# Kernel optimization log

Hardware: AMD Instinct MI355X
Metric: run time of the kernel (lower is better)

Reference implementation:

```python
import jax, jax.numpy as jnp
import numpy as np
import math

N = 25000      # nodes
E = 400000     # edges
L = 2          # GAT layers
H = 8          # heads
DM = 384       # d_model
DE = 64        # d_edge
C = DM // H    # per-head out channels (48)
NB = 41        # gaussian basis: int(8.0/0.2)+1
CUTOFF = 8.0
STEP = 0.2


def setup_inputs():
    key = jax.random.key(0)
    ks = jax.random.split(key, 24)
    s = 0.05
    inp = {
        'x': jax.random.randint(ks[0], (N,), 0, 100, dtype=jnp.int32),
        'edge_index': jax.random.randint(ks[1], (2, E), 0, N, dtype=jnp.int32),
        'edge_attr': jax.random.uniform(ks[2], (E,), dtype=jnp.float32) * CUTOFF,
        'lut': jax.random.normal(ks[3], (100, DM), dtype=jnp.float32) * s,
        'We0': jax.random.normal(ks[4], (NB, DE), dtype=jnp.float32) * s,
        'be0': jnp.zeros((DE,), dtype=jnp.float32),
        'Wl': jax.random.normal(ks[5], (L, DM, DM), dtype=jnp.float32) * s,
        'bl': jnp.zeros((L, DM), dtype=jnp.float32),
        'Wr': jax.random.normal(ks[6], (L, DM, DM), dtype=jnp.float32) * s,
        'br': jnp.zeros((L, DM), dtype=jnp.float32),
        'We': jax.random.normal(ks[7], (L, DE, DM), dtype=jnp.float32) * s,
        'att': jax.random.normal(ks[8], (L, H, C), dtype=jnp.float32) * s,
        'Wres': jax.random.normal(ks[9], (L, DM, DM), dtype=jnp.float32) * s,
        'bias_g': jnp.zeros((L, DM), dtype=jnp.float32),
        'ln_g': jnp.ones((L, DM), dtype=jnp.float32),
        'ln_b': jnp.zeros((L, DM), dtype=jnp.float32),
        'bn_g': jnp.ones((DM,), dtype=jnp.float32),
        'bn_b': jnp.zeros((DM,), dtype=jnp.float32),
    }
    return inp


def _forward(x, edge_index, edge_attr, lut, We0, be0, Wl, bl, Wr, br, We,
             att, Wres, bias_g, ln_g, ln_b, bn_g, bn_b):
    # atom embedding (scaled)
    h = lut[x] * jnp.asarray(math.sqrt(DM), lut.dtype)  # [N, DM]

    # GaussianBasis + edge embedding
    values = jnp.linspace(0.0, CUTOFF, NB, dtype=edge_attr.dtype)
    diff = (edge_attr[:, None] - values) / STEP                 # [E, NB]
    basis = jnp.exp(-(diff * diff)) / 1.12
    ea = basis @ We0 + be0                                      # [E, DE]

    src0, tgt0 = edge_index[0], edge_index[1]
    # add_self_loops with fill_value='mean': scatter-mean of edge_attr at target
    cnt = jax.ops.segment_sum(jnp.ones((E,), ea.dtype), tgt0, num_segments=N)
    sums = jax.ops.segment_sum(ea, tgt0, num_segments=N)
    loop_attr = sums / jnp.maximum(cnt, 1.0)[:, None]           # [N, DE]

    loop = jnp.arange(N, dtype=src0.dtype)
    src = jnp.concatenate([src0, loop])                          # [Et]
    tgt = jnp.concatenate([tgt0, loop])
    ea_full = jnp.concatenate([ea, loop_attr], axis=0)           # [Et, DE]
    Et = E + N

    for l in range(L):
        xl = h @ Wl[l] + bl[l]                                  # [N, DM]
        xr = h @ Wr[l] + br[l]
        e_proj = ea_full @ We[l]                                # [Et, DM]
        m = (xl[src] + xr[tgt] + e_proj).reshape(Et, H, C)
        m = jax.nn.leaky_relu(m, 0.2)
        alpha = jnp.einsum('ehc,hc->eh', m, att[l])             # [Et, H]
        # segment softmax over target nodes (every node has a self-loop)
        amax = jax.ops.segment_max(alpha, tgt, num_segments=N)
        alpha = jnp.exp(alpha - amax[tgt])
        denom = jax.ops.segment_sum(alpha, tgt, num_segments=N)
        alpha = alpha / (denom[tgt] + 1e-16)
        msg = xl[src].reshape(Et, H, C) * alpha[:, :, None]
        out = jax.ops.segment_sum(msg, tgt, num_segments=N).reshape(N, DM)
        out = out + h @ Wres[l] + bias_g[l]                     # residual + bias
        # LayerNorm
        mu = out.mean(axis=-1, keepdims=True)
        var = out.var(axis=-1, keepdims=True)
        h = (out - mu) * jax.lax.rsqrt(var + 1e-5) * ln_g[l] + ln_b[l]

    # BatchNorm1d (training mode: batch stats, biased variance)
    mu = h.mean(axis=0)
    var = h.var(axis=0)
    h = (h - mu) * jax.lax.rsqrt(var + 1e-5) * bn_g + bn_b
    return h


def reference(x, edge_index, edge_attr, lut, We0, be0, Wl, bl, Wr, br, We,
              att, Wres, bias_g, ln_g, ln_b, bn_g, bn_b):
    return _forward(x, edge_index, edge_attr, lut, We0, be0, Wl, bl, Wr, br,
                    We, att, Wres, bias_g, ln_g, ln_b, bn_g, bn_b)
```

## Files before the change

### kernel.cpp

```cpp
#include <hip/hip_runtime.h>
#include <hip/hip_fp16.h>

#define DMv 384
#define DEv 64

typedef __attribute__((ext_vector_type(8))) __bf16 bf16x8;
typedef __attribute__((ext_vector_type(4))) float f32x4;
typedef _Float16 hf16x2 __attribute__((ext_vector_type(2)));

__device__ __forceinline__ float bf_lo(unsigned u){ return __uint_as_float(u << 16); }
__device__ __forceinline__ float bf_hi(unsigned u){ return __uint_as_float(u & 0xffff0000u); }
__device__ __forceinline__ unsigned short f2bf(float f){
  unsigned u = __float_as_uint(f);
  unsigned r = (u + 0x7fffu + ((u >> 16) & 1u)) >> 16;
  return (unsigned short)r;
}
__device__ __forceinline__ float bf2f(unsigned short s){ return __uint_as_float(((unsigned)s) << 16); }

__device__ __forceinline__ unsigned packh2(float a, float b){
  unsigned short ha = __half_as_ushort(__float2half(a));
  unsigned short hb = __half_as_ushort(__float2half(b));
  return (unsigned)ha | ((unsigned)hb << 16);
}
__device__ __forceinline__ float h_lo(unsigned u){ return __half2float(__ushort_as_half((unsigned short)(u & 0xffffu))); }
__device__ __forceinline__ float h_hi(unsigned u){ return __half2float(__ushort_as_half((unsigned short)(u >> 16))); }
__device__ __forceinline__ hf16x2 u2h(unsigned u){ union { unsigned u; hf16x2 h; } x; x.u = u; return x.h; }
__device__ __forceinline__ float dot2(unsigned a, unsigned b, float c){
  return __builtin_amdgcn_fdot2(u2h(a), u2h(b), c, false);
}

__device__ __forceinline__ int phi_col(int c){
  int cp = c >> 1, l = cp / 3, m = cp - 3*l;
  return ((l + (m << 6)) << 1) | (c & 1);
}

__global__ void embed_k(const int* __restrict__ x, const float* __restrict__ lut,
                        unsigned short* __restrict__ hbf) {
  int n = blockIdx.x, c = threadIdx.x;
  hbf[(size_t)n*DMv + c] = f2bf(lut[(size_t)x[n]*DMv + c] * 19.595917942265423f);
}

__global__ void w2_k(const float* __restrict__ We0, const float* __restrict__ be0,
                     const float* __restrict__ We, float* __restrict__ W2,
                     float* __restrict__ bias2) {
  int k = blockIdx.x;
  int l = blockIdx.y;
  int j = threadIdx.x;
  const float* Wel = We + (size_t)l*DEv*DMv;
  if (k == 48) {
    float s = 0.f;
    for (int c = 0; c < DEv; ++c) s = fmaf(be0[c], Wel[c*DMv + j], s);
    bias2[l*DMv + j] = s;
    return;
  }
  float s = 0.f;
  if (k < 41) {
    for (int c = 0; c < DEv; ++c) s = fmaf(We0[k*DEv + c], Wel[c*DMv + j], s);
  }
  W2[((size_t)l*48 + k)*DMv + j] = s;
}

__global__ void w2p_k(const float* __restrict__ W2, unsigned* __restrict__ W2P) {
  int p = blockIdx.x;
  int l = blockIdx.y;
  int c = threadIdx.x;
  const float* base = W2 + (size_t)l*48*DMv;
  float a = base[(2*p)*DMv + c];
  float b = base[(2*p+1)*DMv + c];
  W2P[((size_t)l*24 + p)*DMv + phi_col(c)] = packh2(a, b);
}

__global__ void wcat_k(const float* __restrict__ Wl, const float* __restrict__ Wr,
                       const float* __restrict__ Wres, unsigned short* __restrict__ WcatT) {
  int n = blockIdx.x;
  int l = blockIdx.y;
  int k = threadIdx.x;
  const float* src;
  int nn;
  if (n < 384)      { src = Wl   + (size_t)l*DMv*DMv; nn = n; }
  else if (n < 768) { src = Wr   + (size_t)l*DMv*DMv; nn = n - 384; }
  else              { src = Wres + (size_t)l*DMv*DMv; nn = n - 768; }
  WcatT[((size_t)l*1152 + n)*DMv + k] = f2bf(src[(size_t)k*DMv + nn]);
}

__global__ void bas8_k(const float* __restrict__ edge_attr,
                       uint4* __restrict__ bas8, int* __restrict__ ofs, int Ecnt) {
  int e = blockIdx.x*256 + threadIdx.x;
  if (e >= Ecnt) return;
  float d = edge_attr[e];
  int kc = (int)(d*5.0f + 0.5f);
  int s = (kc - 2) & ~3;
  if (s < 0) s = 0;
  float v[8];
  #pragma unroll
  for (int i = 0; i < 8; ++i) {
    float df = (d - 0.2f*(float)(s+i)) * 5.0f;
    v[i] = __expf(-(df*df)) * (1.0f/1.12f);
  }
  uint4 u;
  u.x = packh2(v[0], v[1]);
  u.y = packh2(v[2], v[3]);
  u.z = packh2(v[4], v[5]);
  u.w = packh2(v[6], v[7]);
  bas8[e] = u;
  ofs[e] = s;
}

__global__ void count_k(const int* __restrict__ tgt, int* __restrict__ cnt, int Ecnt) {
  int e = blockIdx.x*256 + threadIdx.x;
  if (e < Ecnt) atomicAdd(&cnt[tgt[e]], 1);
}
__global__ void scan1_k(const int* __restrict__ cnt, int* __restrict__ rowptr,
                        int* __restrict__ bsum, int n) {
  __shared__ int tmp[256];
  int tid = threadIdx.x, i = blockIdx.x*256 + tid;
  int v = (i < n) ? cnt[i] : 0;
  tmp[tid] = v; __syncthreads();
  for (int off = 1; off < 256; off <<= 1) {
    int xv = (tid >= off) ? tmp[tid-off] : 0;
    __syncthreads();
    tmp[tid] += xv;
    __syncthreads();
  }
  if (i < n) rowptr[i] = tmp[tid] - v;
  if (tid == 255) bsum[blockIdx.x] = tmp[255];
}
__global__ void scan2_k(const int* __restrict__ bsum, int* __restrict__ bsumx, int nb) {
  __shared__ int tmp[256];
  int tid = threadIdx.x;
  int v = (tid < nb) ? bsum[tid] : 0;
  tmp[tid] = v; __syncthreads();
  for (int off = 1; off < 256; off <<= 1) {
    int xv = (tid >= off) ? tmp[tid-off] : 0;
    __syncthreads();
    tmp[tid] += xv;
    __syncthreads();
  }
  bsumx[tid] = tmp[tid] - v;
}
__global__ void scan3_k(int* __restrict__ rowptr, const int* __restrict__ bsumx,
                        int n, int total) {
  int i = blockIdx.x*256 + threadIdx.x;
  if (i < n) rowptr[i] += bsumx[blockIdx.x];
  if (i == 0) rowptr[n] = total;
}
__global__ void fill_k(const int* __restrict__ srcs, const int* __restrict__ tgt,
                       const int* __restrict__ rowptr, int* __restrict__ fill,
                       const uint4* __restrict__ bas8, const int* __restrict__ ofs,
                       int* __restrict__ srcc,
                       uint4* __restrict__ bas8c, int* __restrict__ ofsc, int Ecnt) {
  int e = blockIdx.x*256 + threadIdx.x;
  if (e >= Ecnt) return;
  int t = tgt[e];
  int pos = rowptr[t] + atomicAdd(&fill[t], 1);
  srcc[pos] = srcs[e];
  ofsc[pos] = ofs[e];
  bas8c[pos] = bas8[e];
}

__global__ void mb_k(const uint4* __restrict__ bas8c, const int* __restrict__ ofsc,
                     const int* __restrict__ rowptr,
                     unsigned* __restrict__ mbpk, int Nn) {
  __shared__ float mbS[4][48];
  int tid = threadIdx.x, lane = tid & 63, wv = tid >> 6;
  int t = blockIdx.x*4 + wv;
  if (t >= Nn) return;
  if (lane < 48) mbS[wv][lane] = 0.f;
  asm volatile("s_waitcnt lgkmcnt(0)" ::: "memory");
  int rp = rowptr[t], deg = rowptr[t+1] - rp;
  for (int base = 0; base < deg; base += 64) {
    int i = base + lane;
    if (i < deg) {
      uint4 bu = bas8c[rp + i];
      int s = ofsc[rp + i];
      atomicAdd(&mbS[wv][s+0], h_lo(bu.x));
      atomicAdd(&mbS[wv][s+1], h_hi(bu.x));
      atomicAdd(&mbS[wv][s+2], h_lo(bu.y));
      atomicAdd(&mbS[wv][s+3], h_hi(bu.y));
      atomicAdd(&mbS[wv][s+4], h_lo(bu.z));
      atomicAdd(&mbS[wv][s+5], h_hi(bu.z));
      atomicAdd(&mbS[wv][s+6], h_lo(bu.w));
      atomicAdd(&mbS[wv][s+7], h_hi(bu.w));
    }
  }
  asm volatile("s_waitcnt lgkmcnt(0)" ::: "memory");
  if (lane < 24) {
    float inv = (deg > 0) ? 1.0f / (float)deg : 0.f;
    float a = (2*lane   < 44) ? mbS[wv][2*lane  ] * inv : 0.f;
    float b = (2*lane+1 < 44) ? mbS[wv][2*lane+1] * inv : 0.f;
    mbpk[(size_t)t*24 + lane] = packh2(a, b);
  }
}

__global__ __launch_bounds__(256) void mfma_cat_k(
    const unsigned short* __restrict__ Abf,
    const unsigned short* __restrict__ Bt,
    const float* __restrict__ b0, const float* __restrict__ b1, const float* __restrict__ b2,
    unsigned* __restrict__ C0h, float* __restrict__ C1, float* __restrict__ C2, int M) {
  __shared__ __align__(16) char smem[64*132*4];
  unsigned short* As = (unsigned short*)smem;
  unsigned short* Bs = (unsigned short*)(smem + 16384);
  float* Cs = (float*)smem;
  int tid = threadIdx.x;
  int lane = tid & 63, wv = tid >> 6;
  int wr = wv >> 1, wc = wv & 1;
  int bn = blockIdx.x * 128;
  int bm = blockIdx.y * 128;
  int srow = tid >> 3;
  int scol = (tid & 7) * 8;
  f32x4 acc[4][4] = {};
  uint4 av[4], bv[4];
  #pragma unroll
  for (int c = 0; c < 4; ++c) {
    int gr = bm + c*32 + srow; if (gr >= M) gr = M - 1;
    av[c] = *(const uint4*)(Abf + (size_t)gr*DMv + scol);
    bv[c] = *(const uint4*)(Bt + (size_t)(bn + c*32 + srow)*DMv + scol);
  }
  #pragma unroll
  for (int kt = 0; kt < 6; ++kt) {
    __syncthreads();
    #pragma unroll
    for (int c = 0; c < 4; ++c) {
      int r = c*32 + srow;
      int byteA = r*128 + scol*2;
      byteA ^= ((byteA >> 9) & 1) << 5;
      *(uint4*)((char*)As + byteA) = av[c];
      *(uint4*)((char*)Bs + byteA) = bv[c];
    }
    __syncthreads();
    if (kt < 5) {
      int k0 = (kt+1) * 64;
      #pragma unroll
      for (int c = 0; c < 4; ++c) {
        int gr = bm + c*32 + srow; if (gr >= M) gr = M - 1;
        av[c] = *(const uint4*)(Abf + (size_t)gr*DMv + k0 + scol);
        bv[c] = *(const uint4*)(Bt + (size_t)(bn + c*32 + srow)*DMv + k0 + scol);
      }
    }
    #pragma unroll
    for (int ks = 0; ks < 2; ++ks) {
      bf16x8 af[4], bfv[4];
      #pragma unroll
      for (int m = 0; m < 4; ++m) {
        int r = wr*64 + m*16 + (lane & 15);
        int byte = r*128 + ks*64 + ((lane >> 4)*16);
        byte ^= ((byte >> 9) & 1) << 5;
        af[m] = *(const bf16x8*)((const char*)As + byte);
      }
      #pragma unroll
      for (int n = 0; n < 4; ++n) {
        int r = wc*64 + n*16 + (lane & 15);
        int byte = r*128 + ks*64 + ((lane >> 4)*16);
        byte ^= ((byte >> 9) & 1) << 5;
        bfv[n] = *(const bf16x8*)((const char*)Bs + byte);
      }
      #pragma unroll
      for (int m = 0; m < 4; ++m)
        #pragma unroll
        for (int n = 0; n < 4; ++n)
          acc[m][n] = __builtin_amdgcn_mfma_f32_16x16x32_bf16(af[m], bfv[n], acc[m][n], 0, 0, 0);
    }
  }
  int seg = bn / 384;
  const float* bias = (seg == 0) ? b0 : (seg == 1) ? b1 : b2;
  float* C = (seg == 1) ? C1 : C2;
  int cbase = bn - seg*384;
  #pragma unroll
  for (int half = 0; half < 2; ++half) {
    __syncthreads();
    if (wr == half) {
      #pragma unroll
      for (int m = 0; m < 4; ++m) {
        int rl = m*16 + ((lane >> 4)*4);
        #pragma unroll
        for (int n = 0; n < 4; ++n) {
          int cl = wc*64 + n*16 + (lane & 15);
          #pragma unroll
          for (int q = 0; q < 4; ++q)
            Cs[(rl+q)*132 + cl] = acc[m][n][q];
        }
      }
    }
    __syncthreads();
    #pragma unroll
    for (int rep = 0; rep < 8; ++rep) {
      int rl = rep*8 + (tid >> 5);
      int c4 = (tid & 31) * 4;
      int gr = bm + half*64 + rl;
      if (gr < M) {
        float4 v = *(const float4*)&Cs[rl*132 + c4];
        float4 bv4 = *(const float4*)(bias + cbase + c4);
        v.x += bv4.x; v.y += bv4.y; v.z += bv4.z; v.w += bv4.w;
        if (seg == 0) {
          uint2 pk;
          pk.x = packh2(v.x, v.y);
          pk.y = packh2(v.z, v.w);
          *(uint2*)(C0h + (size_t)gr*192 + ((cbase + c4) >> 1)) = pk;
        } else {
          *(float4*)(C + (size_t)gr*DMv + cbase + c4) = v;
        }
      }
    }
  }
}

__global__ __launch_bounds__(256) void fused_agg_k(
    const unsigned* __restrict__ xlh, const float* __restrict__ xr,
    const float* __restrict__ hres,
    const uint4* __restrict__ bas8c, const int* __restrict__ ofsc,
    const int* __restrict__ srcc, const int* __restrict__ rowptr,
    const unsigned* __restrict__ mbpk,
    const unsigned* __restrict__ W2Pg, const float* __restrict__ bias2_l,
    const float* __restrict__ att_l,
    const float* __restrict__ ln_g, const float* __restrict__ ln_b,
    unsigned short* __restrict__ hbf, int Nn) {
  __shared__ unsigned W2P[24 * DMv];
  int tid = threadIdx.x;
  for (int i = tid; i < 24*DMv; i += 256) W2P[i] = W2Pg[i];
  __syncthreads();
  int lane = tid & 63, wv = tid >> 6;
  int j0 = lane * 6;
  float att_j[6], b2[6], lg[6], lb[6];
  #pragma unroll
  for (int jj = 0; jj < 6; ++jj) {
    att_j[jj] = att_l[j0 + jj];
    b2[jj]    = bias2_l[j0 + jj];
    lg[jj]    = ln_g[j0 + jj];
    lb[jj]    = ln_b[j0 + jj];
  }
  int wgid = blockIdx.x*4 + wv;
  for (int it = 0; it < 4; ++it) {
    int t = wgid*4 + it;
    if (t >= Nn) break;
    int rp = rowptr[t], deg = rowptr[t+1] - rp;
    const float* yp = xr + (size_t)t*DMv + j0;
    float2 c0 = ((const float2*)yp)[0], c1 = ((const float2*)yp)[1], c2 = ((const float2*)yp)[2];
    float xrr[6] = {c0.x, c0.y, c1.x, c1.y, c2.x, c2.y};
    float xrb[6];
    #pragma unroll
    for (int jj = 0; jj < 6; ++jj) xrb[jj] = xrr[jj] + b2[jj];
    float S = 0.f;
    float acc[6] = {0.f,0.f,0.f,0.f,0.f,0.f};
    int r_src = 0, r_ofs = 0; uint4 r_bu = {0,0,0,0};
    if (deg > 0 && lane < 8) {
      int idx = lane; if (idx >= deg) idx = deg - 1;
      int p = rp + idx;
      r_src = srcc[p]; r_bu = bas8c[p]; r_ofs = ofsc[p];
    }
    for (int base = 0; base < deg; base += 8) {
      int nb = deg - base; if (nb > 8) nb = 8;
      int n_src = 0, n_ofs = 0; uint4 n_bu = {0,0,0,0};
      if (base + 8 < deg && lane < 8) {
        int idx = base + 8 + lane; if (idx >= deg) idx = deg - 1;
        int p = rp + idx;
        n_src = srcc[p]; n_bu = bas8c[p]; n_ofs = ofsc[p];
      }
      float xls[8][6];
      #pragma unroll
      for (int s = 0; s < 8; ++s) {
        int sr = __shfl(r_src, s);
        const unsigned* xp = xlh + (size_t)sr*192 + lane*3;
        unsigned u0 = xp[0], u1 = xp[1], u2 = xp[2];
        xls[s][0]=h_lo(u0); xls[s][1]=h_hi(u0); xls[s][2]=h_lo(u1);
        xls[s][3]=h_hi(u1); xls[s][4]=h_lo(u2); xls[s][5]=h_hi(u2);
      }
      #pragma unroll
      for (int s = 0; s < 8; ++s) {
        if (s >= nb) break;
        int p0 = __shfl(r_ofs, s) >> 1;
        unsigned bq0 = __shfl((int)r_bu.x, s);
        unsigned bq1 = __shfl((int)r_bu.y, s);
        unsigned bq2 = __shfl((int)r_bu.z, s);
        unsigned bq3 = __shfl((int)r_bu.w, s);
        float m6[6];
        #pragma unroll
        for (int jj = 0; jj < 6; ++jj) m6[jj] = xls[s][jj] + xrb[jj];
        const uint2* row0 = (const uint2*)(W2P + (p0 + 0)*DMv);
        const uint2* row1 = (const uint2*)(W2P + (p0 + 1)*DMv);
        const uint2* row2 = (const uint2*)(W2P + (p0 + 2)*DMv);
        const uint2* row3 = (const uint2*)(W2P + (p0 + 3)*DMv);
        #pragma unroll
        for (int m = 0; m < 3; ++m) {
          uint2 w0 = row0[lane + (m << 6)];
          uint2 w1 = row1[lane + (m << 6)];
          uint2 w2 = row2[lane + (m << 6)];
          uint2 w3 = row3[lane + (m << 6)];
          m6[2*m]   = dot2(w0.x, bq0, m6[2*m]);
          m6[2*m+1] = dot2(w0.y, bq0, m6[2*m+1]);
          m6[2*m]   = dot2(w1.x, bq1, m6[2*m]);
          m6[2*m+1] = dot2(w1.y, bq1, m6[2*m+1]);
          m6[2*m]   = dot2(w2.x, bq2, m6[2*m]);
          m6[2*m+1] = dot2(w2.y, bq2, m6[2*m+1]);
          m6[2*m]   = dot2(w3.x, bq3, m6[2*m]);
          m6[2*m+1] = dot2(w3.y, bq3, m6[2*m+1]);
        }
        float part = 0.f;
        #pragma unroll
        for (int jj = 0; jj < 6; ++jj) {
          float vl = (m6[jj] > 0.f) ? m6[jj] : 0.2f*m6[jj];
          part = fmaf(vl, att_j[jj], part);
        }
        part += __shfl_xor(part, 1);
        part += __shfl_xor(part, 2);
        part += __shfl_xor(part, 4);
        float w = __expf(part);
        S += w;
        #pragma unroll
        for (int jj = 0; jj < 6; ++jj) acc[jj] = fmaf(w, xls[s][jj], acc[jj]);
      }
      r_src = n_src; r_bu = n_bu; r_ofs = n_ofs;
    }
    {
      const unsigned* xp = xlh + (size_t)t*192 + lane*3;
      unsigned u0 = xp[0], u1 = xp[1], u2 = xp[2];
      float xlt[6] = {h_lo(u0), h_hi(u0), h_lo(u1), h_hi(u1), h_lo(u2), h_hi(u2)};
      float m6[6];
      #pragma unroll
      for (int jj = 0; jj < 6; ++jj)
        m6[jj] = xlt[jj] + ((deg > 0) ? xrb[jj] : xrr[jj]);
      const uint4* mbp4 = (const uint4*)(mbpk + (size_t)t*24);
      #pragma unroll
      for (int w6 = 0; w6 < 6; ++w6) {
        uint4 bu = mbp4[w6];
        unsigned bq[4] = {bu.x, bu.y, bu.z, bu.w};
        #pragma unroll
        for (int q = 0; q < 4; ++q) {
          const uint2* rowq = (const uint2*)(W2P + (w6*4 + q)*DMv);
          #pragma unroll
          for (int m = 0; m < 3; ++m) {
            uint2 wv2 = rowq[lane + (m << 6)];
            m6[2*m]   = dot2(wv2.x, bq[q], m6[2*m]);
            m6[2*m+1] = dot2(wv2.y, bq[q], m6[2*m+1]);
          }
        }
      }
      float part = 0.f;
      #pragma unroll
      for (int jj = 0; jj < 6; ++jj) {
        float vl = (m6[jj] > 0.f) ? m6[jj] : 0.2f*m6[jj];
        part = fmaf(vl, att_j[jj], part);
      }
      part += __shfl_xor(part, 1);
      part += __shfl_xor(part, 2);
      part += __shfl_xor(part, 4);
      float w = __expf(part);
      S += w;
      #pragma unroll
      for (int jj = 0; jj < 6; ++jj) acc[jj] = fmaf(w, xlt[jj], acc[jj]);
    }
    float inv = 1.0f / (S + 1e-16f);
    const float* hrp = hres + (size_t)t*DMv + j0;
    float outv[6]; float s1 = 0.f, s2 = 0.f;
    #pragma unroll
    for (int jj = 0; jj < 6; ++jj) {
      float o = fmaf(acc[jj], inv, hrp[jj]);
      outv[jj] = o; s1 += o; s2 += o*o;
    }
    #pragma unroll
    for (int m = 1; m < 64; m <<= 1) {
      s1 += __shfl_xor(s1, m);
      s2 += __shfl_xor(s2, m);
    }
    float mu  = s1 * (1.0f/384.0f);
    float var = s2 * (1.0f/384.0f) - mu*mu;
    float rs  = rsqrtf(var + 1e-5f);
    float o0 = (outv[0]-mu)*rs*lg[0] + lb[0];
    float o1 = (outv[1]-mu)*rs*lg[1] + lb[1];
    float o2 = (outv[2]-mu)*rs*lg[2] + lb[2];
    float o3 = (outv[3]-mu)*rs*lg[3] + lb[3];
    float o4 = (outv[4]-mu)*rs*lg[4] + lb[4];
    float o5 = (outv[5]-mu)*rs*lg[5] + lb[5];
    unsigned* hp = (unsigned*)(hbf + (size_t)t*DMv + j0);
    hp[0] = (unsigned)f2bf(o0) | ((unsigned)f2bf(o1) << 16);
    hp[1] = (unsigned)f2bf(o2) | ((unsigned)f2bf(o3) << 16);
    hp[2] = (unsigned)f2bf(o4) | ((unsigned)f2bf(o5) << 16);
  }
}

__global__ void bn_reduce_k(const unsigned short* __restrict__ hbf, float* __restrict__ sums, int Nn) {
  int c = threadIdx.x;
  float s = 0.f, s2 = 0.f;
  for (int r = blockIdx.x; r < Nn; r += gridDim.x) {
    float v = bf2f(hbf[(size_t)r*DMv + c]);
    s += v; s2 += v*v;
  }
  atomicAdd(&sums[c], s);
  atomicAdd(&sums[DMv + c], s2);
}
__global__ void bn_params_k(const float* __restrict__ sums,
                            const float* __restrict__ bn_g, const float* __restrict__ bn_b,
                            float* __restrict__ scsh, int Nn) {
  int c = threadIdx.x;
  float mu  = sums[c] / (float)Nn;
  float var = sums[DMv + c] / (float)Nn - mu*mu;
  float rs  = rsqrtf(var + 1e-5f);
  float sc  = bn_g[c] * rs;
  scsh[c] = sc;
  scsh[DMv + c] = bn_b[c] - mu*sc;
}
__global__ void bn_apply_k(const unsigned short* __restrict__ hbf, const float* __restrict__ scsh,
                           float* __restrict__ out) {
  int c = threadIdx.x; int n = blockIdx.x;
  size_t i = (size_t)n*DMv + c;
  out[i] = fmaf(bf2f(hbf[i]), scsh[c], scsh[DMv + c]);
}

extern "C" void kernel_launch(void* const* d_in, const int* in_sizes, int n_in,
                              void* d_out, int out_size, void* d_ws, size_t ws_size,
                              hipStream_t stream) {
  const int Nn   = in_sizes[0];
  const int Ecnt = in_sizes[2];
  const int*   x         = (const int*)d_in[0];
  const int*   eindex    = (const int*)d_in[1];
  const int*   srcs      = eindex;
  const int*   tgts      = eindex + Ecnt;
  const float* edge_attr = (const float*)d_in[2];
  const float* lut       = (const float*)d_in[3];
  const float* We0       = (const float*)d_in[4];
  const float* be0       = (const float*)d_in[5];
  const float* Wl        = (const float*)d_in[6];
  const float* bl_       = (const float*)d_in[7];
  const float* Wr        = (const float*)d_in[8];
  const float* br_       = (const float*)d_in[9];
  const float* We        = (const float*)d_in[10];
  const float* att       = (const float*)d_in[11];
  const float* Wres      = (const float*)d_in[12];
  const float* bias_g    = (const float*)d_in[13];
  const float* ln_g      = (const float*)d_in[14];
  const float* ln_b      = (const float*)d_in[15];
  const float* bn_g      = (const float*)d_in[16];
  const float* bn_b      = (const float*)d_in[17];

  char* ws = (char*)d_ws;
  size_t off = 0;
  auto alloc = [&](size_t b) { size_t o = off; off += (b + 255) & ~(size_t)255; return o; };
  unsigned short* hbf   = (unsigned short*)(ws + alloc((size_t)Nn*DMv*2));
  unsigned* xlh = (unsigned*)(ws + alloc((size_t)Nn*192*4));
  float* xrB   = (float*)(ws + alloc((size_t)Nn*DMv*4));
  float* hresB = (float*)(ws + alloc((size_t)Nn*DMv*4));
  unsigned* mbpk = (unsigned*)(ws + alloc((size_t)Nn*24*4));
  uint4* bas8  = (uint4*)(ws + alloc((size_t)Ecnt*16));
  int* ofs     = (int*)(ws + alloc((size_t)Ecnt*4));
  uint4* bas8c = (uint4*)(ws + alloc((size_t)Ecnt*16));
  int* ofsc    = (int*)(ws + alloc((size_t)Ecnt*4));
  int* srcc    = (int*)(ws + alloc((size_t)Ecnt*4));
  float* W2    = (float*)(ws + alloc((size_t)2*48*DMv*4));
  unsigned* W2P = (unsigned*)(ws + alloc((size_t)2*24*DMv*4));
  float* bias2 = (float*)(ws + alloc((size_t)2*DMv*4));
  unsigned short* WcatT = (unsigned short*)(ws + alloc((size_t)2*1152*DMv*2));
  int* rowptr  = (int*)(ws + alloc((size_t)(Nn+1)*4));
  int* cnt     = (int*)(ws + alloc((size_t)Nn*4));
  int* fillA   = (int*)(ws + alloc((size_t)Nn*4));
  int* bsum    = (int*)(ws + alloc(1024));
  int* bsumx   = (int*)(ws + alloc(1024));
  float* bnsum = (float*)(ws + alloc(2*DMv*4));
  float* scsh  = (float*)(ws + alloc(2*DMv*4));

  hipMemsetAsync(cnt,   0, (size_t)Nn*4, stream);
  hipMemsetAsync(fillA, 0, (size_t)Nn*4, stream);
  hipMemsetAsync(bnsum, 0, 2*DMv*4, stream);

  embed_k<<<Nn, DMv, 0, stream>>>(x, lut, hbf);
  w2_k<<<dim3(49, 2), DMv, 0, stream>>>(We0, be0, We, W2, bias2);
  w2p_k<<<dim3(24, 2), DMv, 0, stream>>>(W2, W2P);
  wcat_k<<<dim3(1152, 2), DMv, 0, stream>>>(Wl, Wr, Wres, WcatT);
  bas8_k<<<(Ecnt+255)/256, 256, 0, stream>>>(edge_attr, bas8, ofs, Ecnt);
  count_k<<<(Ecnt+255)/256, 256, 0, stream>>>(tgts, cnt, Ecnt);
  int nblk = (Nn + 255)/256;
  scan1_k<<<nblk, 256, 0, stream>>>(cnt, rowptr, bsum, Nn);
  scan2_k<<<1, 256, 0, stream>>>(bsum, bsumx, nblk);
  scan3_k<<<nblk, 256, 0, stream>>>(rowptr, bsumx, Nn, Ecnt);
  fill_k<<<(Ecnt+255)/256, 256, 0, stream>>>(srcs, tgts, rowptr, fillA,
                                             bas8, ofs, srcc, bas8c, ofsc, Ecnt);
  mb_k<<<(Nn+3)/4, 256, 0, stream>>>(bas8c, ofsc, rowptr, mbpk, Nn);

  for (int l = 0; l < 2; ++l) {
    mfma_cat_k<<<dim3(9, (Nn+127)/128), 256, 0, stream>>>(
        hbf, WcatT + (size_t)l*1152*DMv,
        bl_ + (size_t)l*DMv, br_ + (size_t)l*DMv, bias_g + (size_t)l*DMv,
        xlh, xrB, hresB, Nn);
    fused_agg_k<<<(Nn+15)/16, 256, 0, stream>>>(
        xlh, xrB, hresB, bas8c, ofsc, srcc, rowptr, mbpk,
        W2P + (size_t)l*24*DMv, bias2 + (size_t)l*DMv, att + (size_t)l*DMv,
        ln_g + (size_t)l*DMv, ln_b + (size_t)l*DMv, hbf, Nn);
  }
  bn_reduce_k<<<200, DMv, 0, stream>>>(hbf, bnsum, Nn);
  bn_params_k<<<1, DMv, 0, stream>>>(bnsum, bn_g, bn_b, scsh, Nn);
  bn_apply_k<<<Nn, DMv, 0, stream>>>(hbf, scsh, (float*)d_out);
}
```

Measured before the change: 714.4 us.

## Store xr and residual GEMM outputs as fp16 and fold memsets into kernels

The GEMM epilogue now packs all three output segments (xl, xr, residual) to fp16 instead of writing xr and the residual as fp32. The aggregation kernel reads and unpacks them, halving intermediate write and read traffic per layer. The three memsets are also removed: zeroing of cnt, fillA and bnsum moves into embed_k, count_k and mb_k. This cuts launch overhead, at the cost of fp16 rounding of xr and the residual before LayerNorm.

```diff
diff --git a/kernel.cpp b/kernel.cpp
--- a/kernel.cpp
+++ b/kernel.cpp
@@ -35,8 +35,9 @@
 }
 
 __global__ void embed_k(const int* __restrict__ x, const float* __restrict__ lut,
-                        unsigned short* __restrict__ hbf) {
+                        unsigned short* __restrict__ hbf, int* __restrict__ cnt) {
   int n = blockIdx.x, c = threadIdx.x;
+  if (c == 0) cnt[n] = 0;
   hbf[(size_t)n*DMv + c] = f2bf(lut[(size_t)x[n]*DMv + c] * 19.595917942265423f);
 }
 
@@ -106,8 +107,10 @@
   ofs[e] = s;
 }
 
-__global__ void count_k(const int* __restrict__ tgt, int* __restrict__ cnt, int Ecnt) {
+__global__ void count_k(const int* __restrict__ tgt, int* __restrict__ cnt,
+                        int* __restrict__ fillA, int Ecnt, int Nn) {
   int e = blockIdx.x*256 + threadIdx.x;
+  if (e < Nn) fillA[e] = 0;
   if (e < Ecnt) atomicAdd(&cnt[tgt[e]], 1);
 }
 __global__ void scan1_k(const int* __restrict__ cnt, int* __restrict__ rowptr,
@@ -160,9 +163,11 @@
 
 __global__ void mb_k(const uint4* __restrict__ bas8c, const int* __restrict__ ofsc,
                      const int* __restrict__ rowptr,
-                     unsigned* __restrict__ mbpk, int Nn) {
+                     unsigned* __restrict__ mbpk, float* __restrict__ bnsum, int Nn) {
   __shared__ float mbS[4][48];
   int tid = threadIdx.x, lane = tid & 63, wv = tid >> 6;
+  int gid = blockIdx.x*256 + tid;
+  if (gid < 2*DMv) bnsum[gid] = 0.f;
   int t = blockIdx.x*4 + wv;
   if (t >= Nn) return;
   if (lane < 48) mbS[wv][lane] = 0.f;
@@ -196,7 +201,7 @@
     const unsigned short* __restrict__ Abf,
     const unsigned short* __restrict__ Bt,
     const float* __restrict__ b0, const float* __restrict__ b1, const float* __restrict__ b2,
-    unsigned* __restrict__ C0h, float* __restrict__ C1, float* __restrict__ C2, int M) {
+    unsigned* __restrict__ C0h, unsigned* __restrict__ C1h, unsigned* __restrict__ C2h, int M) {
   __shared__ __align__(16) char smem[64*132*4];
   unsigned short* As = (unsigned short*)smem;
   unsigned short* Bs = (unsigned short*)(smem + 16384);
@@ -263,7 +268,7 @@
   }
   int seg = bn / 384;
   const float* bias = (seg == 0) ? b0 : (seg == 1) ? b1 : b2;
-  float* C = (seg == 1) ? C1 : C2;
+  unsigned* C = (seg == 0) ? C0h : (seg == 1) ? C1h : C2h;
   int cbase = bn - seg*384;
   #pragma unroll
   for (int half = 0; half < 2; ++half) {
@@ -291,22 +296,18 @@
         float4 v = *(const float4*)&Cs[rl*132 + c4];
         float4 bv4 = *(const float4*)(bias + cbase + c4);
         v.x += bv4.x; v.y += bv4.y; v.z += bv4.z; v.w += bv4.w;
-        if (seg == 0) {
-          uint2 pk;
-          pk.x = packh2(v.x, v.y);
-          pk.y = packh2(v.z, v.w);
-          *(uint2*)(C0h + (size_t)gr*192 + ((cbase + c4) >> 1)) = pk;
-        } else {
-          *(float4*)(C + (size_t)gr*DMv + cbase + c4) = v;
-        }
+        uint2 pk;
+        pk.x = packh2(v.x, v.y);
+        pk.y = packh2(v.z, v.w);
+        *(uint2*)(C + (size_t)gr*192 + ((cbase + c4) >> 1)) = pk;
       }
     }
   }
 }
 
 __global__ __launch_bounds__(256) void fused_agg_k(
-    const unsigned* __restrict__ xlh, const float* __restrict__ xr,
-    const float* __restrict__ hres,
+    const unsigned* __restrict__ xlh, const unsigned* __restrict__ xrh,
+    const unsigned* __restrict__ hresh,
     const uint4* __restrict__ bas8c, const int* __restrict__ ofsc,
     const int* __restrict__ srcc, const int* __restrict__ rowptr,
     const unsigned* __restrict__ mbpk,
@@ -333,9 +334,9 @@
     int t = wgid*4 + it;
     if (t >= Nn) break;
     int rp = rowptr[t], deg = rowptr[t+1] - rp;
-    const float* yp = xr + (size_t)t*DMv + j0;
-    float2 c0 = ((const float2*)yp)[0], c1 = ((const float2*)yp)[1], c2 = ((const float2*)yp)[2];
-    float xrr[6] = {c0.x, c0.y, c1.x, c1.y, c2.x, c2.y};
+    const unsigned* yp = xrh + (size_t)t*192 + lane*3;
+    unsigned y0 = yp[0], y1 = yp[1], y2 = yp[2];
+    float xrr[6] = {h_lo(y0), h_hi(y0), h_lo(y1), h_hi(y1), h_lo(y2), h_hi(y2)};
     float xrb[6];
     #pragma unroll
     for (int jj = 0; jj < 6; ++jj) xrb[jj] = xrr[jj] + b2[jj];
@@ -449,11 +450,13 @@
       for (int jj = 0; jj < 6; ++jj) acc[jj] = fmaf(w, xlt[jj], acc[jj]);
     }
     float inv = 1.0f / (S + 1e-16f);
-    const float* hrp = hres + (size_t)t*DMv + j0;
+    const unsigned* hq = hresh + (size_t)t*192 + lane*3;
+    unsigned hh0 = hq[0], hh1 = hq[1], hh2 = hq[2];
+    float hr[6] = {h_lo(hh0), h_hi(hh0), h_lo(hh1), h_hi(hh1), h_lo(hh2), h_hi(hh2)};
     float outv[6]; float s1 = 0.f, s2 = 0.f;
     #pragma unroll
     for (int jj = 0; jj < 6; ++jj) {
-      float o = fmaf(acc[jj], inv, hrp[jj]);
+      float o = fmaf(acc[jj], inv, hr[jj]);
       outv[jj] = o; s1 += o; s2 += o*o;
     }
     #pragma unroll
@@ -535,9 +538,9 @@
   size_t off = 0;
   auto alloc = [&](size_t b) { size_t o = off; off += (b + 255) & ~(size_t)255; return o; };
   unsigned short* hbf   = (unsigned short*)(ws + alloc((size_t)Nn*DMv*2));
-  unsigned* xlh = (unsigned*)(ws + alloc((size_t)Nn*192*4));
-  float* xrB   = (float*)(ws + alloc((size_t)Nn*DMv*4));
-  float* hresB = (float*)(ws + alloc((size_t)Nn*DMv*4));
+  unsigned* xlh   = (unsigned*)(ws + alloc((size_t)Nn*192*4));
+  unsigned* xrh   = (unsigned*)(ws + alloc((size_t)Nn*192*4));
+  unsigned* hresh = (unsigned*)(ws + alloc((size_t)Nn*192*4));
   unsigned* mbpk = (unsigned*)(ws + alloc((size_t)Nn*24*4));
   uint4* bas8  = (uint4*)(ws + alloc((size_t)Ecnt*16));
   int* ofs     = (int*)(ws + alloc((size_t)Ecnt*4));
@@ -556,31 +559,27 @@
   float* bnsum = (float*)(ws + alloc(2*DMv*4));
   float* scsh  = (float*)(ws + alloc(2*DMv*4));
 
-  hipMemsetAsync(cnt,   0, (size_t)Nn*4, stream);
-  hipMemsetAsync(fillA, 0, (size_t)Nn*4, stream);
-  hipMemsetAsync(bnsum, 0, 2*DMv*4, stream);
-
-  embed_k<<<Nn, DMv, 0, stream>>>(x, lut, hbf);
+  embed_k<<<Nn, DMv, 0, stream>>>(x, lut, hbf, cnt);
   w2_k<<<dim3(49, 2), DMv, 0, stream>>>(We0, be0, We, W2, bias2);
   w2p_k<<<dim3(24, 2), DMv, 0, stream>>>(W2, W2P);
   wcat_k<<<dim3(1152, 2), DMv, 0, stream>>>(Wl, Wr, Wres, WcatT);
   bas8_k<<<(Ecnt+255)/256, 256, 0, stream>>>(edge_attr, bas8, ofs, Ecnt);
-  count_k<<<(Ecnt+255)/256, 256, 0, stream>>>(tgts, cnt, Ecnt);
+  count_k<<<(Ecnt+255)/256, 256, 0, stream>>>(tgts, cnt, fillA, Ecnt, Nn);
   int nblk = (Nn + 255)/256;
   scan1_k<<<nblk, 256, 0, stream>>>(cnt, rowptr, bsum, Nn);
   scan2_k<<<1, 256, 0, stream>>>(bsum, bsumx, nblk);
   scan3_k<<<nblk, 256, 0, stream>>>(rowptr, bsumx, Nn, Ecnt);
   fill_k<<<(Ecnt+255)/256, 256, 0, stream>>>(srcs, tgts, rowptr, fillA,
                                              bas8, ofs, srcc, bas8c, ofsc, Ecnt);
-  mb_k<<<(Nn+3)/4, 256, 0, stream>>>(bas8c, ofsc, rowptr, mbpk, Nn);
+  mb_k<<<(Nn+3)/4, 256, 0, stream>>>(bas8c, ofsc, rowptr, mbpk, bnsum, Nn);
 
   for (int l = 0; l < 2; ++l) {
     mfma_cat_k<<<dim3(9, (Nn+127)/128), 256, 0, stream>>>(
         hbf, WcatT + (size_t)l*1152*DMv,
         bl_ + (size_t)l*DMv, br_ + (size_t)l*DMv, bias_g + (size_t)l*DMv,
-        xlh, xrB, hresB, Nn);
+        xlh, xrh, hresh, Nn);
     fused_agg_k<<<(Nn+15)/16, 256, 0, stream>>>(
-        xlh, xrB, hresB, bas8c, ofsc, srcc, rowptr, mbpk,
+        xlh, xrh, hresh, bas8c, ofsc, srcc, rowptr, mbpk,
         W2P + (size_t)l*24*DMv, bias2 + (size_t)l*DMv, att + (size_t)l*DMv,
         ln_g + (size_t)l*DMv, ln_b + (size_t)l*DMv, hbf, Nn);
   }
```

Measured after the change: 700.0 us. 2.0% less time.
